# Kernel optimization log

Measured on AMD Instinct MI355X. Metric: run time of the kernel, lower is better.

Reference implementation:

```python
import jax, jax.numpy as jnp
import numpy as np

B, L, D = 4, 512, 768
NUM_SPANS = 4096
MAX_WIDTH = 8
DFF = 4 * D


def setup_inputs() -> dict:
    key = jax.random.key(0)
    k_h, k_s, k_w, k1, k2 = jax.random.split(key, 5)
    h = jax.random.normal(k_h, (B, L, D), dtype=jnp.float32)
    starts = jax.random.randint(k_s, (B, NUM_SPANS), 0, L)
    widths = jax.random.randint(k_w, (B, NUM_SPANS), 1, MAX_WIDTH + 1)
    ends = jnp.minimum(starts + widths - 1, L - 1)
    span_idx = jnp.stack([starts, ends], axis=-1).astype(jnp.int64 if jax.config.jax_enable_x64 else jnp.int32)
    W1 = jax.random.normal(k1, (D, DFF), dtype=jnp.float32) * (1.0 / np.sqrt(D))
    b1 = jnp.zeros((DFF,), dtype=jnp.float32)
    W2 = jax.random.normal(k2, (DFF, D), dtype=jnp.float32) * (1.0 / np.sqrt(DFF))
    b2 = jnp.zeros((D,), dtype=jnp.float32)
    return {"h": h, "span_idx": span_idx, "W1": W1, "b1": b1, "W2": W2, "b2": b2,
            "max_width": MAX_WIDTH}


def reference(h, span_idx, W1, b1, W2, b2, max_width):
    # h: [B, L, D]; span_idx: [B, S, 2] (start, end inclusive)
    Bv, Lv, Dv = h.shape
    starts = span_idx[:, :, 0]                       # [B, S]
    lengths = span_idx[:, :, 1] - starts + 1         # [B, S]
    offsets = jnp.arange(max_width)                  # static bound on span length
    positions = starts[:, :, None] + offsets[None, None, :]      # [B, S, W]
    mask = offsets[None, None, :] < lengths[:, :, None]          # [B, S, W]
    positions = jnp.clip(positions * mask, 0, Lv - 1)
    # indexed gather-reduce (no [B,S,L,D] broadcast): [B, S, W, D]
    gathered = h[jnp.arange(Bv)[:, None, None], positions]
    summed = jnp.sum(gathered * mask[..., None].astype(h.dtype), axis=2)  # [B, S, D]
    span_reps = summed / lengths[..., None].astype(h.dtype)
    # projection: Linear -> ReLU -> (Dropout: identity at eval) -> Linear
    hmid = jax.nn.relu(jnp.einsum('bsd,df->bsf', span_reps, W1) + b1)
    out = jnp.einsum('bsf,fd->bsd', hmid, W2) + b2
    return out
```

## Files before the change

kernel.cpp:

```cpp
#include <hip/hip_runtime.h>
#include <stdint.h>

#define B_DIM 4
#define L_DIM 512
#define D_DIM 768
#define S_DIM 4096
#define DFF_DIM 3072
#define M_DIM (B_DIM * S_DIM)

typedef unsigned short ushort_t;
typedef __attribute__((ext_vector_type(8))) short short8;
typedef __attribute__((ext_vector_type(4))) float floatx4;

__device__ __forceinline__ ushort_t f2bf(float x) {
  unsigned int u = __float_as_uint(x);
  u += 0x7FFFu + ((u >> 16) & 1u);
  return (ushort_t)(u >> 16);
}

__device__ __forceinline__ void load_lds16(const ushort_t* g, ushort_t* lds) {
  __builtin_amdgcn_global_load_lds(
      (const __attribute__((address_space(1))) unsigned int*)g,
      (__attribute__((address_space(3))) unsigned int*)lds, 16, 0, 0);
}

__device__ __forceinline__ void transpose_body(const float* __restrict__ in,
                                               ushort_t* __restrict__ out,
                                               int K, int N, int kb, int nb) {
  __shared__ float tile[32][33];
  const int k0 = kb * 32;
  const int n0 = nb * 32;
  const int tx = threadIdx.x & 31;
  const int ty = threadIdx.x >> 5;
#pragma unroll
  for (int r = 0; r < 32; r += 8)
    tile[ty + r][tx] = in[(long)(k0 + ty + r) * N + n0 + tx];
  __syncthreads();
#pragma unroll
  for (int r = 0; r < 32; r += 8)
    out[(long)(n0 + ty + r) * K + k0 + tx] = f2bf(tile[tx][ty + r]);
}

__device__ __forceinline__ void span_body(const float* __restrict__ h,
                                          const int* __restrict__ span_idx,
                                          ushort_t* __restrict__ A, int blk) {
  const int wave = threadIdx.x >> 6;
  const int lane = threadIdx.x & 63;
  const int span = blk * 4 + wave;
  const int b = span >> 12;
  const int start = span_idx[span * 2 + 0];
  const int end   = span_idx[span * 2 + 1];
  const float inv = 1.0f / (float)(end - start + 1);
  const float* hb = h + ((long)b * L_DIM + start) * D_DIM + lane;
  float a[12];
#pragma unroll
  for (int c = 0; c < 12; ++c) a[c] = 0.0f;
  for (int p = start; p <= end; ++p) {
#pragma unroll
    for (int c = 0; c < 12; ++c) a[c] += hb[c * 64];
    hb += D_DIM;
  }
  ushort_t* o = A + (long)span * D_DIM + lane;
#pragma unroll
  for (int c = 0; c < 12; ++c) o[c * 64] = f2bf(a[c] * inv);
}

__global__ __launch_bounds__(256)
void prep(const float* __restrict__ W1, ushort_t* __restrict__ W1T,
          const float* __restrict__ W2, ushort_t* __restrict__ W2T,
          const float* __restrict__ h, const int* __restrict__ span_idx,
          ushort_t* __restrict__ A) {
  const int blk = blockIdx.x;
  if (blk < 2304) {
    transpose_body(W1, W1T, D_DIM, DFF_DIM, blk % 24, blk / 24);
  } else if (blk < 4608) {
    const int b = blk - 2304;
    transpose_body(W2, W2T, DFF_DIM, D_DIM, b % 96, b / 96);
  } else {
    span_body(h, span_idx, A, blk - 4608);
  }
}

template <int MODE>
__global__ __launch_bounds__(256)
void gemm_bt(const ushort_t* __restrict__ A, const ushort_t* __restrict__ Bt,
             const float* __restrict__ bias, void* __restrict__ Cv,
             int M, int N, int K) {
  __shared__ ushort_t As[2][128 * 32];
  __shared__ ushort_t Bs[2][128 * 32];

  const int tid  = threadIdx.x;
  const int lane = tid & 63;
  const int wave = tid >> 6;
  const int l16  = lane & 15;
  const int quad = lane >> 4;

  const int bm = blockIdx.x;
  const int bn = blockIdx.y;

  const int wm = (wave & 1) * 64;
  const int wn = (wave >> 1) * 64;

  const int swz  = (l16 & 3) ^ ((l16 >> 2) & 3);
  const int coff = (quad ^ swz) * 8;

  floatx4 acc[4][4];
#pragma unroll
  for (int i = 0; i < 4; ++i)
#pragma unroll
    for (int j = 0; j < 4; ++j)
      acc[i][j] = (floatx4)0.0f;

  const int s0 = tid, s1 = tid + 256;
  const int r0 = s0 >> 2, r1 = s1 >> 2;
  const int c0 = (s0 & 3) ^ (r0 & 3) ^ ((r0 >> 2) & 3);
  const int c1 = (s1 & 3) ^ (r1 & 3) ^ ((r1 >> 2) & 3);
  const ushort_t* gA0 = A + (long)(bm * 128 + r0) * K + c0 * 8;
  const ushort_t* gA1 = A + (long)(bm * 128 + r1) * K + c1 * 8;
  const ushort_t* gB0 = Bt + (long)(bn * 128 + r0) * K + c0 * 8;
  const ushort_t* gB1 = Bt + (long)(bn * 128 + r1) * K + c1 * 8;

  const int nk = K >> 5;

  load_lds16(gA0, &As[0][0] + s0 * 8);
  load_lds16(gA1, &As[0][0] + s1 * 8);
  load_lds16(gB0, &Bs[0][0] + s0 * 8);
  load_lds16(gB1, &Bs[0][0] + s1 * 8);

  for (int k = 0; k < nk; ++k) {
    const int cur = k & 1;
    const int nxt = cur ^ 1;
    __syncthreads();

    if (k + 1 < nk) {
      const int off = (k + 1) * 32;
      load_lds16(gA0 + off, &As[nxt][0] + s0 * 8);
      load_lds16(gA1 + off, &As[nxt][0] + s1 * 8);
      load_lds16(gB0 + off, &Bs[nxt][0] + s0 * 8);
      load_lds16(gB1 + off, &Bs[nxt][0] + s1 * 8);
    }

    short8 af[4], bf[4];
#pragma unroll
    for (int i = 0; i < 4; ++i)
      af[i] = *(const short8*)(&As[cur][0] + (wm + i * 16 + l16) * 32 + coff);
#pragma unroll
    for (int j = 0; j < 4; ++j)
      bf[j] = *(const short8*)(&Bs[cur][0] + (wn + j * 16 + l16) * 32 + coff);
#pragma unroll
    for (int i = 0; i < 4; ++i)
#pragma unroll
      for (int j = 0; j < 4; ++j)
        acc[i][j] = __builtin_amdgcn_mfma_f32_16x16x32_bf16(af[i], bf[j], acc[i][j], 0, 0, 0);
  }

#pragma unroll
  for (int i = 0; i < 4; ++i) {
#pragma unroll
    for (int j = 0; j < 4; ++j) {
      const int col = bn * 128 + wn + j * 16 + l16;
      const float bv = bias[col];
      const int row0 = bm * 128 + wm + i * 16 + quad * 4;
#pragma unroll
      for (int r = 0; r < 4; ++r) {
        float v = acc[i][j][r] + bv;
        if (MODE == 0) {
          v = v > 0.0f ? v : 0.0f;
          ((ushort_t*)Cv)[(long)(row0 + r) * N + col] = f2bf(v);
        } else {
          ((float*)Cv)[(long)(row0 + r) * N + col] = v;
        }
      }
    }
  }
}

extern "C" void kernel_launch(void* const* d_in, const int* in_sizes, int n_in,
                              void* d_out, int out_size, void* d_ws, size_t ws_size,
                              hipStream_t stream) {
  const float* h        = (const float*)d_in[0];
  const int*   span_idx = (const int*)d_in[1];
  const float* W1       = (const float*)d_in[2];
  const float* b1       = (const float*)d_in[3];
  const float* W2       = (const float*)d_in[4];
  const float* b2       = (const float*)d_in[5];
  float* out = (float*)d_out;

  ushort_t* A   = (ushort_t*)d_ws;
  ushort_t* W1T = A + (size_t)M_DIM * D_DIM;
  ushort_t* W2T = W1T + (size_t)DFF_DIM * D_DIM;
  ushort_t* Hm  = W2T + (size_t)D_DIM * DFF_DIM;

  prep<<<2304 + 2304 + M_DIM / 4, 256, 0, stream>>>(W1, W1T, W2, W2T, h, span_idx, A);

  gemm_bt<0><<<dim3(M_DIM / 128, DFF_DIM / 128), 256, 0, stream>>>(
      A, W1T, b1, Hm, M_DIM, DFF_DIM, D_DIM);

  gemm_bt<1><<<dim3(M_DIM / 128, D_DIM / 128), 256, 0, stream>>>(
      Hm, W2T, b2, out, M_DIM, D_DIM, DFF_DIM);
}
```

Before: 279.2 us.

## Load B fragments directly to registers and drop the B LDS buffer

The GEMM now reads each wave's B-operand fragments straight from global memory into registers, double-buffered across two register sets, and keeps only A staged in LDS. The K loop is unrolled by two with explicit ping-pong buffers, and the XOR swizzle on the A tile is removed. This cuts LDS traffic and footprint, which may allow higher occupancy. In exchange, B loads are no longer shared between the waves that need the same columns, so global and L2 traffic rises, and the unswizzled A reads may hit LDS bank conflicts.

```diff
diff --git a/kernel.cpp b/kernel.cpp
--- a/kernel.cpp
+++ b/kernel.cpp
@@ -87,7 +87,6 @@
              const float* __restrict__ bias, void* __restrict__ Cv,
              int M, int N, int K) {
   __shared__ ushort_t As[2][128 * 32];
-  __shared__ ushort_t Bs[2][128 * 32];
 
   const int tid  = threadIdx.x;
   const int lane = tid & 63;
@@ -101,9 +100,6 @@
   const int wm = (wave & 1) * 64;
   const int wn = (wave >> 1) * 64;
 
-  const int swz  = (l16 & 3) ^ ((l16 >> 2) & 3);
-  const int coff = (quad ^ swz) * 8;
-
   floatx4 acc[4][4];
 #pragma unroll
   for (int i = 0; i < 4; ++i)
@@ -111,47 +107,65 @@
     for (int j = 0; j < 4; ++j)
       acc[i][j] = (floatx4)0.0f;
 
-  const int s0 = tid, s1 = tid + 256;
-  const int r0 = s0 >> 2, r1 = s1 >> 2;
-  const int c0 = (s0 & 3) ^ (r0 & 3) ^ ((r0 >> 2) & 3);
-  const int c1 = (s1 & 3) ^ (r1 & 3) ^ ((r1 >> 2) & 3);
-  const ushort_t* gA0 = A + (long)(bm * 128 + r0) * K + c0 * 8;
-  const ushort_t* gA1 = A + (long)(bm * 128 + r1) * K + c1 * 8;
-  const ushort_t* gB0 = Bt + (long)(bn * 128 + r0) * K + c0 * 8;
-  const ushort_t* gB1 = Bt + (long)(bn * 128 + r1) * K + c1 * 8;
+  const int s0 = tid;
+  const ushort_t* gA0 = A + (long)(bm * 128 + (s0 >> 2)) * K + (s0 & 3) * 8;
+  const long a1off = (long)64 * K;
+
+  const ushort_t* gB = Bt + (long)(bn * 128 + wn + l16) * K + quad * 8;
+  const long jstride = (long)16 * K;
 
   const int nk = K >> 5;
 
+  short8 b0[4], b1[4];
+
   load_lds16(gA0, &As[0][0] + s0 * 8);
-  load_lds16(gA1, &As[0][0] + s1 * 8);
-  load_lds16(gB0, &Bs[0][0] + s0 * 8);
-  load_lds16(gB1, &Bs[0][0] + s1 * 8);
-
-  for (int k = 0; k < nk; ++k) {
-    const int cur = k & 1;
-    const int nxt = cur ^ 1;
+  load_lds16(gA0 + a1off, &As[0][0] + s0 * 8 + 2048);
+#pragma unroll
+  for (int j = 0; j < 4; ++j)
+    b0[j] = *(const short8*)(gB + j * jstride);
+
+  for (int kk = 0; kk < nk; kk += 2) {
     __syncthreads();
-
-    if (k + 1 < nk) {
-      const int off = (k + 1) * 32;
-      load_lds16(gA0 + off, &As[nxt][0] + s0 * 8);
-      load_lds16(gA1 + off, &As[nxt][0] + s1 * 8);
-      load_lds16(gB0 + off, &Bs[nxt][0] + s0 * 8);
-      load_lds16(gB1 + off, &Bs[nxt][0] + s1 * 8);
-    }
-
-    short8 af[4], bf[4];
-#pragma unroll
-    for (int i = 0; i < 4; ++i)
-      af[i] = *(const short8*)(&As[cur][0] + (wm + i * 16 + l16) * 32 + coff);
-#pragma unroll
-    for (int j = 0; j < 4; ++j)
-      bf[j] = *(const short8*)(&Bs[cur][0] + (wn + j * 16 + l16) * 32 + coff);
-#pragma unroll
-    for (int i = 0; i < 4; ++i)
+    {
+      const int off = (kk + 1) * 32;
+      load_lds16(gA0 + off, &As[1][0] + s0 * 8);
+      load_lds16(gA0 + a1off + off, &As[1][0] + s0 * 8 + 2048);
 #pragma unroll
       for (int j = 0; j < 4; ++j)
-        acc[i][j] = __builtin_amdgcn_mfma_f32_16x16x32_bf16(af[i], bf[j], acc[i][j], 0, 0, 0);
+        b1[j] = *(const short8*)(gB + j * jstride + off);
+    }
+    {
+      short8 af[4];
+#pragma unroll
+      for (int i = 0; i < 4; ++i)
+        af[i] = *(const short8*)(&As[0][0] + (wm + i * 16 + l16) * 32 + quad * 8);
+#pragma unroll
+      for (int i = 0; i < 4; ++i)
+#pragma unroll
+        for (int j = 0; j < 4; ++j)
+          acc[i][j] = __builtin_amdgcn_mfma_f32_16x16x32_bf16(af[i], b0[j], acc[i][j], 0, 0, 0);
+    }
+
+    __syncthreads();
+    if (kk + 2 < nk) {
+      const int off = (kk + 2) * 32;
+      load_lds16(gA0 + off, &As[0][0] + s0 * 8);
+      load_lds16(gA0 + a1off + off, &As[0][0] + s0 * 8 + 2048);
+#pragma unroll
+      for (int j = 0; j < 4; ++j)
+        b0[j] = *(const short8*)(gB + j * jstride + off);
+    }
+    {
+      short8 af[4];
+#pragma unroll
+      for (int i = 0; i < 4; ++i)
+        af[i] = *(const short8*)(&As[1][0] + (wm + i * 16 + l16) * 32 + quad * 8);
+#pragma unroll
+      for (int i = 0; i < 4; ++i)
+#pragma unroll
+        for (int j = 0; j < 4; ++j)
+          acc[i][j] = __builtin_amdgcn_mfma_f32_16x16x32_bf16(af[i], b1[j], acc[i][j], 0, 0, 0);
+    }
   }
 
 #pragma unroll
```

Result: slower. 485.8 us (+74.0%).

## Enlarge GEMM block tile to 256x256 and drop LDS XOR swizzle

Applied to the files above, without the earlier changes.

The block tile of both bf16 MFMA GEMMs grows from 128x128 to 256x256, so each wave computes a 128x128 sub-tile with an 8x8 grid of accumulators. Launch bounds are set to one block per SIMD group, which allows the much larger register footprint. The goal is more data reuse per LDS load and less global traffic per FLOP. In exchange, the LDS swizzle is removed, which risks bank conflicts on the fragment reads; the grids get much smaller (64x3 blocks for the second GEMM); and 256 accumulator VGPRs per lane risk spills and low occupancy.

```diff
diff --git a/kernel.cpp b/kernel.cpp
--- a/kernel.cpp
+++ b/kernel.cpp
@@ -82,12 +82,12 @@
 }
 
 template <int MODE>
-__global__ __launch_bounds__(256)
+__global__ __launch_bounds__(256, 1)
 void gemm_bt(const ushort_t* __restrict__ A, const ushort_t* __restrict__ Bt,
              const float* __restrict__ bias, void* __restrict__ Cv,
              int M, int N, int K) {
-  __shared__ ushort_t As[2][128 * 32];
-  __shared__ ushort_t Bs[2][128 * 32];
+  __shared__ ushort_t As[2][256 * 32];
+  __shared__ ushort_t Bs[2][256 * 32];
 
   const int tid  = threadIdx.x;
   const int lane = tid & 63;
@@ -98,34 +98,27 @@
   const int bm = blockIdx.x;
   const int bn = blockIdx.y;
 
-  const int wm = (wave & 1) * 64;
-  const int wn = (wave >> 1) * 64;
+  const int wm = (wave & 1) * 128;
+  const int wn = (wave >> 1) * 128;
 
-  const int swz  = (l16 & 3) ^ ((l16 >> 2) & 3);
-  const int coff = (quad ^ swz) * 8;
-
-  floatx4 acc[4][4];
+  floatx4 acc[8][8];
 #pragma unroll
-  for (int i = 0; i < 4; ++i)
+  for (int i = 0; i < 8; ++i)
 #pragma unroll
-    for (int j = 0; j < 4; ++j)
+    for (int j = 0; j < 8; ++j)
       acc[i][j] = (floatx4)0.0f;
 
-  const int s0 = tid, s1 = tid + 256;
-  const int r0 = s0 >> 2, r1 = s1 >> 2;
-  const int c0 = (s0 & 3) ^ (r0 & 3) ^ ((r0 >> 2) & 3);
-  const int c1 = (s1 & 3) ^ (r1 & 3) ^ ((r1 >> 2) & 3);
-  const ushort_t* gA0 = A + (long)(bm * 128 + r0) * K + c0 * 8;
-  const ushort_t* gA1 = A + (long)(bm * 128 + r1) * K + c1 * 8;
-  const ushort_t* gB0 = Bt + (long)(bn * 128 + r0) * K + c0 * 8;
-  const ushort_t* gB1 = Bt + (long)(bn * 128 + r1) * K + c1 * 8;
+  const ushort_t* gA0 = A + (long)(bm * 256 + (tid >> 2)) * K + (tid & 3) * 8;
+  const ushort_t* gB0 = Bt + (long)(bn * 256 + (tid >> 2)) * K + (tid & 3) * 8;
+  const long rstep = (long)64 * K;
 
   const int nk = K >> 5;
 
-  load_lds16(gA0, &As[0][0] + s0 * 8);
-  load_lds16(gA1, &As[0][0] + s1 * 8);
-  load_lds16(gB0, &Bs[0][0] + s0 * 8);
-  load_lds16(gB1, &Bs[0][0] + s1 * 8);
+#pragma unroll
+  for (int r = 0; r < 4; ++r) {
+    load_lds16(gA0 + r * rstep, &As[0][0] + tid * 8 + r * 2048);
+    load_lds16(gB0 + r * rstep, &Bs[0][0] + tid * 8 + r * 2048);
+  }
 
   for (int k = 0; k < nk; ++k) {
     const int cur = k & 1;
@@ -134,33 +127,34 @@
 
     if (k + 1 < nk) {
       const int off = (k + 1) * 32;
-      load_lds16(gA0 + off, &As[nxt][0] + s0 * 8);
-      load_lds16(gA1 + off, &As[nxt][0] + s1 * 8);
-      load_lds16(gB0 + off, &Bs[nxt][0] + s0 * 8);
-      load_lds16(gB1 + off, &Bs[nxt][0] + s1 * 8);
+#pragma unroll
+      for (int r = 0; r < 4; ++r) {
+        load_lds16(gA0 + r * rstep + off, &As[nxt][0] + tid * 8 + r * 2048);
+        load_lds16(gB0 + r * rstep + off, &Bs[nxt][0] + tid * 8 + r * 2048);
+      }
     }
 
-    short8 af[4], bf[4];
+    short8 af[8], bf[8];
 #pragma unroll
-    for (int i = 0; i < 4; ++i)
-      af[i] = *(const short8*)(&As[cur][0] + (wm + i * 16 + l16) * 32 + coff);
+    for (int i = 0; i < 8; ++i)
+      af[i] = *(const short8*)(&As[cur][0] + (wm + i * 16 + l16) * 32 + quad * 8);
 #pragma unroll
-    for (int j = 0; j < 4; ++j)
-      bf[j] = *(const short8*)(&Bs[cur][0] + (wn + j * 16 + l16) * 32 + coff);
+    for (int j = 0; j < 8; ++j)
+      bf[j] = *(const short8*)(&Bs[cur][0] + (wn + j * 16 + l16) * 32 + quad * 8);
 #pragma unroll
-    for (int i = 0; i < 4; ++i)
+    for (int i = 0; i < 8; ++i)
 #pragma unroll
-      for (int j = 0; j < 4; ++j)
+      for (int j = 0; j < 8; ++j)
         acc[i][j] = __builtin_amdgcn_mfma_f32_16x16x32_bf16(af[i], bf[j], acc[i][j], 0, 0, 0);
   }
 
 #pragma unroll
-  for (int i = 0; i < 4; ++i) {
+  for (int i = 0; i < 8; ++i) {
 #pragma unroll
-    for (int j = 0; j < 4; ++j) {
-      const int col = bn * 128 + wn + j * 16 + l16;
+    for (int j = 0; j < 8; ++j) {
+      const int col = bn * 256 + wn + j * 16 + l16;
       const float bv = bias[col];
-      const int row0 = bm * 128 + wm + i * 16 + quad * 4;
+      const int row0 = bm * 256 + wm + i * 16 + quad * 4;
 #pragma unroll
       for (int r = 0; r < 4; ++r) {
         float v = acc[i][j][r] + bv;
@@ -193,9 +187,9 @@
 
   prep<<<2304 + 2304 + M_DIM / 4, 256, 0, stream>>>(W1, W1T, W2, W2T, h, span_idx, A);
 
-  gemm_bt<0><<<dim3(M_DIM / 128, DFF_DIM / 128), 256, 0, stream>>>(
+  gemm_bt<0><<<dim3(M_DIM / 256, DFF_DIM / 256), 256, 0, stream>>>(
       A, W1T, b1, Hm, M_DIM, DFF_DIM, D_DIM);
 
-  gemm_bt<1><<<dim3(M_DIM / 128, D_DIM / 128), 256, 0, stream>>>(
+  gemm_bt<1><<<dim3(M_DIM / 256, D_DIM / 256), 256, 0, stream>>>(
       Hm, W2T, b2, out, M_DIM, D_DIM, DFF_DIM);
 }
```

Result: slower. 377.5 us (+35.2%).

## Apply W1 before span pooling using prefix sums over projected tokens

Applied to the files above, without the earlier changes.

Span mean-pooling is linear, so the first Linear is now run on the 2048 token rows instead of the 16384 span rows. A per-column prefix sum along L is then taken over the fp32 result, and each span's pre-activation is recovered as (P[end+1]-P[start])/len + b1, followed by ReLU. This is meant to cut the first GEMM's FLOPs by about 8x. In exchange it adds a serial 12-block scan kernel, an fp32 intermediate buffer and a bandwidth-heavy gather, and fp32 prefix differences may lose some precision. The LDS XOR swizzle in the GEMM is also removed, which may bring back bank conflicts in the second GEMM.

```diff
diff --git a/kernel.cpp b/kernel.cpp
--- a/kernel.cpp
+++ b/kernel.cpp
@@ -7,9 +7,11 @@
 #define S_DIM 4096
 #define DFF_DIM 3072
 #define M_DIM (B_DIM * S_DIM)
+#define HROWS (B_DIM * L_DIM)
 
 typedef unsigned short ushort_t;
 typedef __attribute__((ext_vector_type(8))) short short8;
+typedef __attribute__((ext_vector_type(8))) ushort_t ushort8;
 typedef __attribute__((ext_vector_type(4))) float floatx4;
 
 __device__ __forceinline__ ushort_t f2bf(float x) {
@@ -41,35 +43,10 @@
     out[(long)(n0 + ty + r) * K + k0 + tx] = f2bf(tile[tx][ty + r]);
 }
 
-__device__ __forceinline__ void span_body(const float* __restrict__ h,
-                                          const int* __restrict__ span_idx,
-                                          ushort_t* __restrict__ A, int blk) {
-  const int wave = threadIdx.x >> 6;
-  const int lane = threadIdx.x & 63;
-  const int span = blk * 4 + wave;
-  const int b = span >> 12;
-  const int start = span_idx[span * 2 + 0];
-  const int end   = span_idx[span * 2 + 1];
-  const float inv = 1.0f / (float)(end - start + 1);
-  const float* hb = h + ((long)b * L_DIM + start) * D_DIM + lane;
-  float a[12];
-#pragma unroll
-  for (int c = 0; c < 12; ++c) a[c] = 0.0f;
-  for (int p = start; p <= end; ++p) {
-#pragma unroll
-    for (int c = 0; c < 12; ++c) a[c] += hb[c * 64];
-    hb += D_DIM;
-  }
-  ushort_t* o = A + (long)span * D_DIM + lane;
-#pragma unroll
-  for (int c = 0; c < 12; ++c) o[c * 64] = f2bf(a[c] * inv);
-}
-
 __global__ __launch_bounds__(256)
 void prep(const float* __restrict__ W1, ushort_t* __restrict__ W1T,
           const float* __restrict__ W2, ushort_t* __restrict__ W2T,
-          const float* __restrict__ h, const int* __restrict__ span_idx,
-          ushort_t* __restrict__ A) {
+          const float* __restrict__ h, ushort_t* __restrict__ Hbf) {
   const int blk = blockIdx.x;
   if (blk < 2304) {
     transpose_body(W1, W1T, D_DIM, DFF_DIM, blk % 24, blk / 24);
@@ -77,8 +54,63 @@
     const int b = blk - 2304;
     transpose_body(W2, W2T, DFF_DIM, D_DIM, b % 96, b / 96);
   } else {
-    span_body(h, span_idx, A, blk - 4608);
-  }
+    const long base = (long)(blk - 4608) * 2048 + threadIdx.x * 8;
+    const float4 v0 = *(const float4*)(h + base);
+    const float4 v1 = *(const float4*)(h + base + 4);
+    ushort8 o;
+    o[0] = f2bf(v0.x); o[1] = f2bf(v0.y); o[2] = f2bf(v0.z); o[3] = f2bf(v0.w);
+    o[4] = f2bf(v1.x); o[5] = f2bf(v1.y); o[6] = f2bf(v1.z); o[7] = f2bf(v1.w);
+    *(ushort8*)(Hbf + base) = o;
+  }
+}
+
+__global__ __launch_bounds__(256)
+void scan_l(const float* __restrict__ HW1, float* __restrict__ P) {
+  const int b  = blockIdx.x / 3;
+  const int cc = blockIdx.x % 3;
+  const int col = cc * 1024 + threadIdx.x * 4;
+  const float* src = HW1 + (long)b * L_DIM * DFF_DIM + col;
+  float* dst = P + (long)b * (L_DIM + 1) * DFF_DIM + col;
+  float4 v = make_float4(0.f, 0.f, 0.f, 0.f);
+  *(float4*)dst = v;
+  for (int l = 0; l < L_DIM; ++l) {
+    const float4 x = *(const float4*)(src + (long)l * DFF_DIM);
+    v.x += x.x; v.y += x.y; v.z += x.z; v.w += x.w;
+    *(float4*)(dst + (long)(l + 1) * DFF_DIM) = v;
+  }
+}
+
+__global__ __launch_bounds__(256)
+void gather_spans(const float* __restrict__ P, const int* __restrict__ span_idx,
+                  const float* __restrict__ b1, ushort_t* __restrict__ Hmid) {
+  const unsigned unit = blockIdx.x * 256 + threadIdx.x;
+  const unsigned span = unit / 384;
+  const unsigned c8   = unit % 384;
+  const int b     = span >> 12;
+  const int start = span_idx[span * 2 + 0];
+  const int end   = span_idx[span * 2 + 1];
+  const float inv = 1.0f / (float)(end - start + 1);
+  const float* pe = P + ((long)b * (L_DIM + 1) + end + 1) * DFF_DIM + c8 * 8;
+  const float* ps = P + ((long)b * (L_DIM + 1) + start) * DFF_DIM + c8 * 8;
+  const float4 e0 = *(const float4*)(pe);
+  const float4 e1 = *(const float4*)(pe + 4);
+  const float4 s0 = *(const float4*)(ps);
+  const float4 s1 = *(const float4*)(ps + 4);
+  const float4 g0 = *(const float4*)(b1 + c8 * 8);
+  const float4 g1 = *(const float4*)(b1 + c8 * 8 + 4);
+  float v[8];
+  v[0] = (e0.x - s0.x) * inv + g0.x;
+  v[1] = (e0.y - s0.y) * inv + g0.y;
+  v[2] = (e0.z - s0.z) * inv + g0.z;
+  v[3] = (e0.w - s0.w) * inv + g0.w;
+  v[4] = (e1.x - s1.x) * inv + g1.x;
+  v[5] = (e1.y - s1.y) * inv + g1.y;
+  v[6] = (e1.z - s1.z) * inv + g1.z;
+  v[7] = (e1.w - s1.w) * inv + g1.w;
+  ushort8 o;
+#pragma unroll
+  for (int i = 0; i < 8; ++i) o[i] = f2bf(v[i] > 0.f ? v[i] : 0.f);
+  *(ushort8*)(Hmid + (long)span * DFF_DIM + c8 * 8) = o;
 }
 
 template <int MODE>
@@ -101,9 +133,6 @@
   const int wm = (wave & 1) * 64;
   const int wn = (wave >> 1) * 64;
 
-  const int swz  = (l16 & 3) ^ ((l16 >> 2) & 3);
-  const int coff = (quad ^ swz) * 8;
-
   floatx4 acc[4][4];
 #pragma unroll
   for (int i = 0; i < 4; ++i)
@@ -112,13 +141,10 @@
       acc[i][j] = (floatx4)0.0f;
 
   const int s0 = tid, s1 = tid + 256;
-  const int r0 = s0 >> 2, r1 = s1 >> 2;
-  const int c0 = (s0 & 3) ^ (r0 & 3) ^ ((r0 >> 2) & 3);
-  const int c1 = (s1 & 3) ^ (r1 & 3) ^ ((r1 >> 2) & 3);
-  const ushort_t* gA0 = A + (long)(bm * 128 + r0) * K + c0 * 8;
-  const ushort_t* gA1 = A + (long)(bm * 128 + r1) * K + c1 * 8;
-  const ushort_t* gB0 = Bt + (long)(bn * 128 + r0) * K + c0 * 8;
-  const ushort_t* gB1 = Bt + (long)(bn * 128 + r1) * K + c1 * 8;
+  const ushort_t* gA0 = A + (long)(bm * 128 + (s0 >> 2)) * K + (s0 & 3) * 8;
+  const ushort_t* gA1 = A + (long)(bm * 128 + (s1 >> 2)) * K + (s1 & 3) * 8;
+  const ushort_t* gB0 = Bt + (long)(bn * 128 + (s0 >> 2)) * K + (s0 & 3) * 8;
+  const ushort_t* gB1 = Bt + (long)(bn * 128 + (s1 >> 2)) * K + (s1 & 3) * 8;
 
   const int nk = K >> 5;
 
@@ -143,10 +169,10 @@
     short8 af[4], bf[4];
 #pragma unroll
     for (int i = 0; i < 4; ++i)
-      af[i] = *(const short8*)(&As[cur][0] + (wm + i * 16 + l16) * 32 + coff);
+      af[i] = *(const short8*)(&As[cur][0] + (wm + i * 16 + l16) * 32 + quad * 8);
 #pragma unroll
     for (int j = 0; j < 4; ++j)
-      bf[j] = *(const short8*)(&Bs[cur][0] + (wn + j * 16 + l16) * 32 + coff);
+      bf[j] = *(const short8*)(&Bs[cur][0] + (wn + j * 16 + l16) * 32 + quad * 8);
 #pragma unroll
     for (int i = 0; i < 4; ++i)
 #pragma unroll
@@ -159,7 +185,7 @@
 #pragma unroll
     for (int j = 0; j < 4; ++j) {
       const int col = bn * 128 + wn + j * 16 + l16;
-      const float bv = bias[col];
+      const float bv = (MODE == 2) ? 0.0f : bias[col];
       const int row0 = bm * 128 + wm + i * 16 + quad * 4;
 #pragma unroll
       for (int r = 0; r < 4; ++r) {
@@ -186,16 +212,25 @@
   const float* b2       = (const float*)d_in[5];
   float* out = (float*)d_out;
 
-  ushort_t* A   = (ushort_t*)d_ws;
-  ushort_t* W1T = A + (size_t)M_DIM * D_DIM;
-  ushort_t* W2T = W1T + (size_t)DFF_DIM * D_DIM;
-  ushort_t* Hm  = W2T + (size_t)D_DIM * DFF_DIM;
-
-  prep<<<2304 + 2304 + M_DIM / 4, 256, 0, stream>>>(W1, W1T, W2, W2T, h, span_idx, A);
-
-  gemm_bt<0><<<dim3(M_DIM / 128, DFF_DIM / 128), 256, 0, stream>>>(
-      A, W1T, b1, Hm, M_DIM, DFF_DIM, D_DIM);
+  char* ws = (char*)d_ws;
+  ushort_t* W2T  = (ushort_t*)ws;
+  float*    P    = (float*)(ws + 4718592);
+  char*     reg  = ws + 29933568;
+  ushort_t* Hmid = (ushort_t*)reg;
+  float*    HW1  = (float*)reg;
+  ushort_t* W1T  = (ushort_t*)(reg + 33554432);
+  ushort_t* Hbf  = (ushort_t*)(reg + 41943040);
+
+  prep<<<2304 + 2304 + 768, 256, 0, stream>>>(W1, W1T, W2, W2T, h, Hbf);
+
+  gemm_bt<2><<<dim3(HROWS / 128, DFF_DIM / 128), 256, 0, stream>>>(
+      Hbf, W1T, nullptr, HW1, HROWS, DFF_DIM, D_DIM);
+
+  scan_l<<<12, 256, 0, stream>>>(HW1, P);
+
+  gather_spans<<<(M_DIM * (DFF_DIM / 8)) / 256, 256, 0, stream>>>(
+      P, span_idx, b1, Hmid);
 
   gemm_bt<1><<<dim3(M_DIM / 128, D_DIM / 128), 256, 0, stream>>>(
-      Hm, W2T, b2, out, M_DIM, D_DIM, DFF_DIM);
-}
+      Hmid, W2T, b2, out, M_DIM, D_DIM, DFF_DIM);
+}
```

Result: slower. 286.7 us (+2.7%).
